# Performance work log

Hardware: AMD Instinct MI355X
Metric: run time of the kernel (lower is better)

## Reference

```python
import jax, jax.numpy as jnp
import numpy as np

N = 50000          # nodes
E = 1600000        # edges (avg degree 32)
D_MODEL = 128      # input == output dim
HEADS = 4
D_HEAD = D_MODEL // HEADS
N_LAYERS = 3


def _edge_softmax(scores, dst, n):
    # scores: [E, H]; softmax over edges sharing the same destination node
    m = jax.ops.segment_max(scores, dst, num_segments=n)          # [N, H]
    m = jnp.where(jnp.isfinite(m), m, 0.0)                        # empty segments -> -inf guard
    ex = jnp.exp(scores - m[dst])                                 # [E, H]
    denom = jax.ops.segment_sum(ex, dst, num_segments=n)          # [N, H]
    return ex / (denom[dst] + 1e-9)


def _gt_layer(h, src, dst, Wq, Wk, Wv, Wo):
    # h: [N, D]; one multi-head graph-attention (graph transformer) layer
    n = h.shape[0]
    q = (h @ Wq).reshape(n, HEADS, D_HEAD)
    k = (h @ Wk).reshape(n, HEADS, D_HEAD)
    v = (h @ Wv).reshape(n, HEADS, D_HEAD)
    scale = 1.0 / np.sqrt(D_HEAD).astype(np.float32)
    scores = jnp.einsum('ehd,ehd->eh', q[dst], k[src]) * scale    # [E, H]
    alpha = _edge_softmax(scores, dst, n)                         # [E, H]
    agg = jax.ops.segment_sum(alpha[:, :, None] * v[src], dst, num_segments=n)  # [N, H, Dh]
    return agg.reshape(n, D_MODEL) @ Wo


def setup_inputs() -> dict:
    key = jax.random.key(0)
    ks = jax.random.split(key, 16)
    s = 1.0 / np.sqrt(D_MODEL)
    inp = {
        'X':    jax.random.normal(ks[0], (N, 1), jnp.float32),
        'Seed': jax.random.uniform(ks[1], (N, 1), jnp.float32),
        'D':    jax.random.uniform(ks[2], (N, 1), jnp.float32),
        'C':    jax.random.uniform(ks[3], (N, 1), jnp.float32),
        'edge_src': jax.random.randint(ks[4], (E,), 0, N, jnp.int32),
        'edge_dst': jax.random.randint(ks[5], (E,), 0, N, jnp.int32),
        # scalar -> d_model embeddings (Linear(1, d, bias=False))
        'W_seed': jax.random.normal(ks[6], (1, D_MODEL), jnp.float32),
        'W_deg':  jax.random.normal(ks[7], (1, D_MODEL), jnp.float32),
        'W_clu':  jax.random.normal(ks[8], (1, D_MODEL), jnp.float32),
        # 3 graph-transformer layers
        'Wq': jax.random.normal(ks[9],  (N_LAYERS, D_MODEL, D_MODEL), jnp.float32) * s,
        'Wk': jax.random.normal(ks[10], (N_LAYERS, D_MODEL, D_MODEL), jnp.float32) * s,
        'Wv': jax.random.normal(ks[11], (N_LAYERS, D_MODEL, D_MODEL), jnp.float32) * s,
        'Wo': jax.random.normal(ks[12], (N_LAYERS, D_MODEL, D_MODEL), jnp.float32) * s,
        # MLP head: Linear(d,d)+ReLU, Linear(d,1)
        'W1': jax.random.normal(ks[13], (D_MODEL, D_MODEL), jnp.float32) * s,
        'b1': jnp.zeros((D_MODEL,), jnp.float32),
        'W2': jax.random.normal(ks[14], (D_MODEL, 1), jnp.float32) * s,
        'b2': jnp.zeros((1,), jnp.float32),
    }
    return inp


def reference(X, Seed, D, C, edge_src, edge_dst,
              W_seed, W_deg, W_clu, Wq, Wk, Wv, Wo, W1, b1, W2, b2):
    # faithful to original: raw X [N,1] broadcast-added to the embeddings
    h = X + Seed @ W_seed + D @ W_deg + C @ W_clu                 # [N, D_MODEL]
    for i in range(N_LAYERS):
        h = _gt_layer(h, edge_src, edge_dst, Wq[i], Wk[i], Wv[i], Wo[i])
    z = jax.nn.relu(h @ W1 + b1)
    return z @ W2 + b2                                            # [N, 1]
```

## Files before the change

### kernel.cpp

```cpp
#include <hip/hip_runtime.h>
#include <math.h>

#define DM 128
#define HEADS 4
#define DH 32
#define WSTRIDE 16384

typedef _Float16 f16x8 __attribute__((ext_vector_type(8)));
typedef _Float16 f16x4 __attribute__((ext_vector_type(4)));
typedef _Float16 f16x2 __attribute__((ext_vector_type(2)));
typedef float f32x4v __attribute__((ext_vector_type(4)));

__device__ __forceinline__ float dpp_xor1_add(float x) {
    int r = __builtin_amdgcn_update_dpp(0, __builtin_bit_cast(int, x), 0xB1, 0xf, 0xf, true);
    return x + __builtin_bit_cast(float, r);
}
__device__ __forceinline__ float dpp_xor2_add(float x) {
    int r = __builtin_amdgcn_update_dpp(0, __builtin_bit_cast(int, x), 0x4E, 0xf, 0xf, true);
    return x + __builtin_bit_cast(float, r);
}

__global__ void embed_kernel(const float* __restrict__ X, const float* __restrict__ Seed,
                             const float* __restrict__ Dg, const float* __restrict__ Cl,
                             const float* __restrict__ Wseed, const float* __restrict__ Wdeg,
                             const float* __restrict__ Wclu, float* __restrict__ H, int n) {
    int i = blockIdx.x * blockDim.x + threadIdx.x;
    if (i >= n * (DM / 4)) return;
    int nd = i >> 5, d4 = (i & 31) * 4;
    float x = X[nd], sd = Seed[nd], dg = Dg[nd], cl = Cl[nd];
    float4 ws = *reinterpret_cast<const float4*>(Wseed + d4);
    float4 wd = *reinterpret_cast<const float4*>(Wdeg + d4);
    float4 wc = *reinterpret_cast<const float4*>(Wclu + d4);
    float4 o;
    o.x = x + sd * ws.x + dg * wd.x + cl * wc.x;
    o.y = x + sd * ws.y + dg * wd.y + cl * wc.y;
    o.z = x + sd * ws.z + dg * wd.z + cl * wc.z;
    o.w = x + sd * ws.w + dg * wd.w + cl * wc.w;
    *reinterpret_cast<float4*>(H + nd * DM + d4) = o;
}

__global__ void count_kernel(const int* __restrict__ edst, int* __restrict__ deg, int E) {
    int e = blockIdx.x * blockDim.x + threadIdx.x;
    if (e < E) atomicAdd(&deg[edst[e]], 1);
}

__global__ void scan1_kernel(const int* __restrict__ in, int* __restrict__ outv,
                             int* __restrict__ bsums, int n) {
    __shared__ int s[256];
    int t = threadIdx.x;
    int i = blockIdx.x * 256 + t;
    int v = (i < n) ? in[i] : 0;
    s[t] = v;
    __syncthreads();
    for (int off = 1; off < 256; off <<= 1) {
        int x = (t >= off) ? s[t - off] : 0;
        __syncthreads();
        s[t] += x;
        __syncthreads();
    }
    if (i < n) outv[i] = s[t];
    if (t == 255) bsums[blockIdx.x] = s[255];
}

__global__ void scan2_kernel(int* __restrict__ bsums, int nb) {
    __shared__ int s[256];
    int t = threadIdx.x;
    int v = (t < nb) ? bsums[t] : 0;
    s[t] = v;
    __syncthreads();
    for (int off = 1; off < 256; off <<= 1) {
        int x = (t >= off) ? s[t - off] : 0;
        __syncthreads();
        s[t] += x;
        __syncthreads();
    }
    if (t < nb) bsums[t] = s[t];
}

__global__ void scan3_kernel(const int* __restrict__ outv, const int* __restrict__ bsums,
                             int* __restrict__ ptr, int n) {
    int i = blockIdx.x * 256 + threadIdx.x;
    if (i == 0) ptr[0] = 0;
    if (i < n) {
        int add = (blockIdx.x > 0) ? bsums[blockIdx.x - 1] : 0;
        ptr[i + 1] = outv[i] + add;
    }
}

__global__ void scatter_kernel(const int* __restrict__ esrc, const int* __restrict__ edst,
                               const int* __restrict__ ptr, int* __restrict__ fill,
                               int* __restrict__ out, int E) {
    int e = blockIdx.x * blockDim.x + threadIdx.x;
    if (e >= E) return;
    int d = edst[e];
    int pos = ptr[d] + atomicAdd(&fill[d], 1);
    out[pos] = esrc[e];
}

__global__ void prepack_kernel(const float* __restrict__ Wq, const float* __restrict__ Wk,
                               const float* __restrict__ Wv, const float* __restrict__ Wo,
                               const float* __restrict__ W1, _Float16* __restrict__ W16) {
    int m = blockIdx.z;
    const float* W;
    if (m < 3)       W = Wq + (size_t)m * DM * DM;
    else if (m < 6)  W = Wk + (size_t)(m - 3) * DM * DM;
    else if (m < 9)  W = Wv + (size_t)(m - 6) * DM * DM;
    else if (m < 12) W = Wo + (size_t)(m - 9) * DM * DM;
    else             W = W1;
    int kb = blockIdx.x, nb = blockIdx.y, l = threadIdx.x;
    int kbase = kb * 32 + (l >> 4) * 8;
    int c = nb * 16 + (l & 15);
    f16x8 v;
#pragma unroll
    for (int j = 0; j < 8; j++) v[j] = (_Float16)W[(kbase + j) * DM + c];
    *reinterpret_cast<f16x8*>(W16 + (size_t)m * WSTRIDE + ((kb * 8 + nb) * 64 + l) * 8) = v;
}

template <int OUT>
__global__ __launch_bounds__(256) void gemm_mfma_kernel(const float* __restrict__ A,
                                                        const _Float16* __restrict__ W16,
                                                        void* __restrict__ O, int ldO,
                                                        int colOff, int n) {
    __shared__ _Float16 sA[64 * 136];
    int t = threadIdx.x;
    int row0 = blockIdx.x * 64;
#pragma unroll
    for (int p = 0; p < 8; p++) {
        int f = p * 256 + t;
        int r = f >> 5, c4 = (f & 31) * 4;
        int gr = min(row0 + r, n - 1);
        float4 v = *reinterpret_cast<const float4*>(A + (size_t)gr * DM + c4);
        f16x4 h = {(_Float16)v.x, (_Float16)v.y, (_Float16)v.z, (_Float16)v.w};
        *reinterpret_cast<f16x4*>(&sA[r * 136 + c4]) = h;
    }
    __syncthreads();

    int w = t >> 6, l = t & 63;
    int lr = l & 15, lg = l >> 4;
    int rowb = w * 16;

    f32x4v acc[8];
#pragma unroll
    for (int nb = 0; nb < 8; nb++) acc[nb] = (f32x4v){0.f, 0.f, 0.f, 0.f};

#pragma unroll
    for (int kb = 0; kb < 4; kb++) {
        f16x8 a = *reinterpret_cast<const f16x8*>(&sA[(rowb + lr) * 136 + kb * 32 + lg * 8]);
#pragma unroll
        for (int nb = 0; nb < 8; nb++) {
            f16x8 b = *reinterpret_cast<const f16x8*>(&W16[((kb * 8 + nb) * 64 + l) * 8]);
            acc[nb] = __builtin_amdgcn_mfma_f32_16x16x32_f16(a, b, acc[nb], 0, 0, 0);
        }
    }

#pragma unroll
    for (int nb = 0; nb < 8; nb++) {
#pragma unroll
        for (int i = 0; i < 4; i++) {
            int r = row0 + rowb + lg * 4 + i;
            if (r >= n) continue;
            int c = nb * 16 + lr;
            if (OUT == 0) {
                ((float*)O)[(size_t)r * ldO + c] = acc[nb][i];
            } else {
                _Float16 h = (_Float16)acc[nb][i];
                ((unsigned short*)O)[(size_t)r * ldO + colOff + c] =
                    __builtin_bit_cast(unsigned short, h);
            }
        }
    }
}

__global__ __launch_bounds__(256) void attn_kernel(const float* __restrict__ Q,
                                                   const uint32_t* __restrict__ KV,
                                                   const int* __restrict__ ptr,
                                                   const int* __restrict__ esrc,
                                                   float* __restrict__ AGG, int n) {
    int wv = threadIdx.x >> 6;
    int lane = threadIdx.x & 63;
    int node = blockIdx.x * 4 + wv;
    if (node >= n) return;
    int e0 = ptr[node], e1 = ptr[node + 1];
    int q4 = lane >> 4;
    int w = lane & 15;
    float* outbase = AGG + (size_t)node * DM + 8 * w;
    if (e0 >= e1) {
        if (lane < 16) {
            *reinterpret_cast<float4*>(outbase) = make_float4(0.f, 0.f, 0.f, 0.f);
            *reinterpret_cast<float4*>(outbase + 4) = make_float4(0.f, 0.f, 0.f, 0.f);
        }
        return;
    }
    const float scale = 0.17677669529663687f * 1.4426950408889634f;
    float4 qa = *reinterpret_cast<const float4*>(Q + (size_t)node * DM + 8 * w);
    float4 qb = *reinterpret_cast<const float4*>(Q + (size_t)node * DM + 8 * w + 4);
    f16x2 qh0 = {(_Float16)(qa.x * scale), (_Float16)(qa.y * scale)};
    f16x2 qh1 = {(_Float16)(qa.z * scale), (_Float16)(qa.w * scale)};
    f16x2 qh2 = {(_Float16)(qb.x * scale), (_Float16)(qb.y * scale)};
    f16x2 qh3 = {(_Float16)(qb.z * scale), (_Float16)(qb.w * scale)};

    float m = -1e30f, s = 0.f;
    float a0 = 0.f, a1 = 0.f, a2 = 0.f, a3 = 0.f, a4 = 0.f, a5 = 0.f, a6 = 0.f, a7 = 0.f;

    int last = e1 - 1;
    int niter = (e1 - e0 + 3) >> 2;
    int niter2 = (niter + 1) >> 1;

    const uint32_t* kvw = KV + w * 4;

    uint4 k0, v0, k1, v1;
    {
        int i0 = esrc[min(e0 + q4, last)];
        const uint32_t* r0 = kvw + (size_t)i0 * 128;
        k0 = *reinterpret_cast<const uint4*>(r0);
        v0 = *reinterpret_cast<const uint4*>(r0 + 64);
        int i1 = esrc[min(e0 + 4 + q4, last)];
        const uint32_t* r1 = kvw + (size_t)i1 * 128;
        k1 = *reinterpret_cast<const uint4*>(r1);
        v1 = *reinterpret_cast<const uint4*>(r1 + 64);
    }
    int idx2 = esrc[min(e0 + 8 + q4, last)];

#define APROC(kc, vc, bidx)                                                            \
    {                                                                                  \
        float p = __builtin_amdgcn_fdot2(qh0, __builtin_bit_cast(f16x2, (kc).x), 0.f, false); \
        p = __builtin_amdgcn_fdot2(qh1, __builtin_bit_cast(f16x2, (kc).y), p, false);  \
        p = __builtin_amdgcn_fdot2(qh2, __builtin_bit_cast(f16x2, (kc).z), p, false);  \
        p = __builtin_amdgcn_fdot2(qh3, __builtin_bit_cast(f16x2, (kc).w), p, false);  \
        p = dpp_xor1_add(p);                                                           \
        p = dpp_xor2_add(p);                                                           \
        p = ((bidx) < e1) ? p : -3.0e38f;                                              \
        float diff = p - m;                                                            \
        if (__any(diff > 8.f)) {                                                       \
            float mn = fmaxf(m, p);                                                    \
            float dd = exp2f(m - mn);                                                  \
            s *= dd;                                                                   \
            a0 *= dd; a1 *= dd; a2 *= dd; a3 *= dd;                                    \
            a4 *= dd; a5 *= dd; a6 *= dd; a7 *= dd;                                    \
            m = mn;                                                                    \
            diff = p - m;                                                              \
        }                                                                              \
        float wg = exp2f(diff);                                                        \
        s += wg;                                                                       \
        f16x2 vh0 = __builtin_bit_cast(f16x2, (vc).x);                                 \
        f16x2 vh1 = __builtin_bit_cast(f16x2, (vc).y);                                 \
        f16x2 vh2 = __builtin_bit_cast(f16x2, (vc).z);                                 \
        f16x2 vh3 = __builtin_bit_cast(f16x2, (vc).w);                                 \
        a0 += wg * (float)vh0[0]; a1 += wg * (float)vh0[1];                            \
        a2 += wg * (float)vh1[0]; a3 += wg * (float)vh1[1];                            \
        a4 += wg * (float)vh2[0]; a5 += wg * (float)vh2[1];                            \
        a6 += wg * (float)vh3[0]; a7 += wg * (float)vh3[1];                            \
    }

    int b = e0 + q4;
    for (int it = 0; it < niter2; it++) {
        {
            uint4 kc = k0, vc = v0;
            const uint32_t* r = kvw + (size_t)idx2 * 128;
            k0 = *reinterpret_cast<const uint4*>(r);
            v0 = *reinterpret_cast<const uint4*>(r + 64);
            idx2 = esrc[min(b + 12, last)];
            APROC(kc, vc, b);
            b += 4;
        }
        {
            uint4 kc = k1, vc = v1;
            const uint32_t* r = kvw + (size_t)idx2 * 128;
            k1 = *reinterpret_cast<const uint4*>(r);
            v1 = *reinterpret_cast<const uint4*>(r + 64);
            idx2 = esrc[min(b + 12, last)];
            APROC(kc, vc, b);
            b += 4;
        }
    }
#undef APROC

#pragma unroll
    for (int off = 16; off <= 32; off <<= 1) {
        float m2 = __shfl_xor(m, off, 64);
        float s2 = __shfl_xor(s, off, 64);
        float b0 = __shfl_xor(a0, off, 64), b1 = __shfl_xor(a1, off, 64);
        float b2 = __shfl_xor(a2, off, 64), b3 = __shfl_xor(a3, off, 64);
        float b4 = __shfl_xor(a4, off, 64), b5 = __shfl_xor(a5, off, 64);
        float b6 = __shfl_xor(a6, off, 64), b7 = __shfl_xor(a7, off, 64);
        float mF = fmaxf(m, m2);
        float d1 = exp2f(m - mF), d2 = exp2f(m2 - mF);
        s = s * d1 + s2 * d2;
        a0 = a0 * d1 + b0 * d2; a1 = a1 * d1 + b1 * d2;
        a2 = a2 * d1 + b2 * d2; a3 = a3 * d1 + b3 * d2;
        a4 = a4 * d1 + b4 * d2; a5 = a5 * d1 + b5 * d2;
        a6 = a6 * d1 + b6 * d2; a7 = a7 * d1 + b7 * d2;
        m = mF;
    }

    float inv = 1.f / (s + 1e-9f);
    if (lane < 16) {
        *reinterpret_cast<float4*>(outbase) =
            make_float4(a0 * inv, a1 * inv, a2 * inv, a3 * inv);
        *reinterpret_cast<float4*>(outbase + 4) =
            make_float4(a4 * inv, a5 * inv, a6 * inv, a7 * inv);
    }
}

__global__ __launch_bounds__(256) void mlp_kernel(const float* __restrict__ H,
                                                  const _Float16* __restrict__ W16,
                                                  const float* __restrict__ b1,
                                                  const float* __restrict__ W2,
                                                  const float* __restrict__ b2,
                                                  float* __restrict__ out, int n) {
    __shared__ _Float16 sA[64 * 136];
    int t = threadIdx.x;
    int row0 = blockIdx.x * 64;
#pragma unroll
    for (int p = 0; p < 8; p++) {
        int f = p * 256 + t;
        int r = f >> 5, c4 = (f & 31) * 4;
        int gr = min(row0 + r, n - 1);
        float4 v = *reinterpret_cast<const float4*>(H + (size_t)gr * DM + c4);
        f16x4 h = {(_Float16)v.x, (_Float16)v.y, (_Float16)v.z, (_Float16)v.w};
        *reinterpret_cast<f16x4*>(&sA[r * 136 + c4]) = h;
    }
    __syncthreads();

    int w = t >> 6, l = t & 63;
    int lr = l & 15, lg = l >> 4;
    int rowb = w * 16;

    f32x4v acc[8];
#pragma unroll
    for (int nb = 0; nb < 8; nb++) acc[nb] = (f32x4v){0.f, 0.f, 0.f, 0.f};

#pragma unroll
    for (int kb = 0; kb < 4; kb++) {
        f16x8 a = *reinterpret_cast<const f16x8*>(&sA[(rowb + lr) * 136 + kb * 32 + lg * 8]);
#pragma unroll
        for (int nb = 0; nb < 8; nb++) {
            f16x8 b = *reinterpret_cast<const f16x8*>(&W16[((kb * 8 + nb) * 64 + l) * 8]);
            acc[nb] = __builtin_amdgcn_mfma_f32_16x16x32_f16(a, b, acc[nb], 0, 0, 0);
        }
    }

    float part[4] = {0.f, 0.f, 0.f, 0.f};
#pragma unroll
    for (int nb = 0; nb < 8; nb++) {
        int c = nb * 16 + lr;
        float b1v = b1[c];
        float w2v = W2[c];
#pragma unroll
        for (int i = 0; i < 4; i++) {
            float z = fmaxf(acc[nb][i] + b1v, 0.f);
            part[i] += z * w2v;
        }
    }
    float b2v = b2[0];
#pragma unroll
    for (int i = 0; i < 4; i++) {
        part[i] += __shfl_xor(part[i], 1, 64);
        part[i] += __shfl_xor(part[i], 2, 64);
        part[i] += __shfl_xor(part[i], 4, 64);
        part[i] += __shfl_xor(part[i], 8, 64);
        int r = row0 + rowb + lg * 4 + i;
        if (lr == 0 && r < n) out[r] = part[i] + b2v;
    }
}

extern "C" void kernel_launch(void* const* d_in, const int* in_sizes, int n_in,
                              void* d_out, int out_size, void* d_ws, size_t ws_size,
                              hipStream_t stream) {
    const float* X    = (const float*)d_in[0];
    const float* Seed = (const float*)d_in[1];
    const float* Dg   = (const float*)d_in[2];
    const float* Cl   = (const float*)d_in[3];
    const int* esrc   = (const int*)d_in[4];
    const int* edst   = (const int*)d_in[5];
    const float* Wseed = (const float*)d_in[6];
    const float* Wdeg  = (const float*)d_in[7];
    const float* Wclu  = (const float*)d_in[8];
    const float* Wq = (const float*)d_in[9];
    const float* Wk = (const float*)d_in[10];
    const float* Wv = (const float*)d_in[11];
    const float* Wo = (const float*)d_in[12];
    const float* W1 = (const float*)d_in[13];
    const float* b1 = (const float*)d_in[14];
    const float* W2 = (const float*)d_in[15];
    const float* b2 = (const float*)d_in[16];
    float* out = (float*)d_out;

    int n = in_sizes[0];
    int E = in_sizes[4];

    char* p = (char*)d_ws;
    auto alloc = [&](size_t bytes) {
        void* r = (void*)p;
        p += (bytes + 255) & ~(size_t)255;
        return r;
    };
    float* hbuf  = (float*)alloc((size_t)n * DM * 4);
    float* qbuf  = (float*)alloc((size_t)n * DM * 4);
    float* abuf  = (float*)alloc((size_t)n * DM * 4);
    unsigned short* kvbuf = (unsigned short*)alloc((size_t)n * 256 * 2);
    _Float16* W16 = (_Float16*)alloc((size_t)13 * WSTRIDE * 2);
    int* deg    = (int*)alloc((size_t)n * 4);
    int* ptr    = (int*)alloc((size_t)(n + 1) * 4);
    int* ptrtmp = (int*)alloc((size_t)n * 4);
    int* bsums  = (int*)alloc(1024);
    int* fill   = (int*)alloc((size_t)n * 4);
    int* esrcs  = (int*)alloc((size_t)E * 4);
    (void)ws_size; (void)n_in; (void)out_size;

    hipMemsetAsync(deg, 0, (size_t)n * 4, stream);
    hipMemsetAsync(fill, 0, (size_t)n * 4, stream);

    {
        int total = n * (DM / 4);
        embed_kernel<<<(total + 255) / 256, 256, 0, stream>>>(X, Seed, Dg, Cl, Wseed, Wdeg,
                                                              Wclu, hbuf, n);
    }
    int nb = (n + 255) / 256;
    count_kernel<<<(E + 255) / 256, 256, 0, stream>>>(edst, deg, E);
    scan1_kernel<<<nb, 256, 0, stream>>>(deg, ptrtmp, bsums, n);
    scan2_kernel<<<1, 256, 0, stream>>>(bsums, nb);
    scan3_kernel<<<nb, 256, 0, stream>>>(ptrtmp, bsums, ptr, n);
    scatter_kernel<<<(E + 255) / 256, 256, 0, stream>>>(esrc, edst, ptr, fill, esrcs, E);

    prepack_kernel<<<dim3(4, 8, 13), 64, 0, stream>>>(Wq, Wk, Wv, Wo, W1, W16);

    int ggrid = (n + 63) / 64;
    int agrid = (n + 3) / 4;
    for (int i = 0; i < 3; i++) {
        const _Float16* wq16 = W16 + (size_t)(0 + i) * WSTRIDE;
        const _Float16* wk16 = W16 + (size_t)(3 + i) * WSTRIDE;
        const _Float16* wv16 = W16 + (size_t)(6 + i) * WSTRIDE;
        const _Float16* wo16 = W16 + (size_t)(9 + i) * WSTRIDE;
        gemm_mfma_kernel<0><<<ggrid, 256, 0, stream>>>(hbuf, wq16, qbuf, DM, 0, n);
        gemm_mfma_kernel<1><<<ggrid, 256, 0, stream>>>(hbuf, wk16, kvbuf, 256, 0, n);
        gemm_mfma_kernel<1><<<ggrid, 256, 0, stream>>>(hbuf, wv16, kvbuf, 256, 128, n);
        attn_kernel<<<agrid, 256, 0, stream>>>(qbuf, (const uint32_t*)kvbuf, ptr, esrcs,
                                               abuf, n);
        gemm_mfma_kernel<0><<<ggrid, 256, 0, stream>>>(abuf, wo16, hbuf, DM, 0, n);
    }
    mlp_kernel<<<ggrid, 256, 0, stream>>>(hbuf, W16 + (size_t)12 * WSTRIDE, b1, W2, b2, out, n);
}
```

Before: 716.9 us.

## Fuse embed/Wo projections with QKV GEMMs and MLP; store activations in fp16

Measured after the change: 670.7 us. -6.5%, faster.

```diff
diff --git a/kernel.cpp b/kernel.cpp
--- a/kernel.cpp
+++ b/kernel.cpp
@@ -19,24 +19,9 @@
     int r = __builtin_amdgcn_update_dpp(0, __builtin_bit_cast(int, x), 0x4E, 0xf, 0xf, true);
     return x + __builtin_bit_cast(float, r);
 }
-
-__global__ void embed_kernel(const float* __restrict__ X, const float* __restrict__ Seed,
-                             const float* __restrict__ Dg, const float* __restrict__ Cl,
-                             const float* __restrict__ Wseed, const float* __restrict__ Wdeg,
-                             const float* __restrict__ Wclu, float* __restrict__ H, int n) {
-    int i = blockIdx.x * blockDim.x + threadIdx.x;
-    if (i >= n * (DM / 4)) return;
-    int nd = i >> 5, d4 = (i & 31) * 4;
-    float x = X[nd], sd = Seed[nd], dg = Dg[nd], cl = Cl[nd];
-    float4 ws = *reinterpret_cast<const float4*>(Wseed + d4);
-    float4 wd = *reinterpret_cast<const float4*>(Wdeg + d4);
-    float4 wc = *reinterpret_cast<const float4*>(Wclu + d4);
-    float4 o;
-    o.x = x + sd * ws.x + dg * wd.x + cl * wc.x;
-    o.y = x + sd * ws.y + dg * wd.y + cl * wc.y;
-    o.z = x + sd * ws.z + dg * wd.z + cl * wc.z;
-    o.w = x + sd * ws.w + dg * wd.w + cl * wc.w;
-    *reinterpret_cast<float4*>(H + nd * DM + d4) = o;
+__device__ __forceinline__ uint32_t pkh(float x, float y) {
+    f16x2 h = {(_Float16)x, (_Float16)y};
+    return __builtin_bit_cast(uint32_t, h);
 }
 
 __global__ void count_kernel(const int* __restrict__ edst, int* __restrict__ deg, int E) {
@@ -116,66 +101,182 @@
     *reinterpret_cast<f16x8*>(W16 + (size_t)m * WSTRIDE + ((kb * 8 + nb) * 64 + l) * 8) = v;
 }
 
-template <int OUT>
-__global__ __launch_bounds__(256) void gemm_mfma_kernel(const float* __restrict__ A,
-                                                        const _Float16* __restrict__ W16,
-                                                        void* __restrict__ O, int ldO,
-                                                        int colOff, int n) {
-    __shared__ _Float16 sA[64 * 136];
+__device__ __forceinline__ void tile_gemm(const _Float16* __restrict__ sRow,
+                                          const _Float16* __restrict__ W16, int lg, int l,
+                                          f32x4v acc[8]) {
+#pragma unroll
+    for (int nb = 0; nb < 8; nb++) acc[nb] = (f32x4v){0.f, 0.f, 0.f, 0.f};
+#pragma unroll
+    for (int kb = 0; kb < 4; kb++) {
+        f16x8 a = *reinterpret_cast<const f16x8*>(sRow + kb * 32 + lg * 8);
+#pragma unroll
+        for (int nb = 0; nb < 8; nb++) {
+            f16x8 b = *reinterpret_cast<const f16x8*>(&W16[((kb * 8 + nb) * 64 + l) * 8]);
+            acc[nb] = __builtin_amdgcn_mfma_f32_16x16x32_f16(a, b, acc[nb], 0, 0, 0);
+        }
+    }
+}
+
+__device__ __forceinline__ void qkv_store(const _Float16* __restrict__ sH, int rowb, int lr,
+                                          int lg, int l, int row0, int n,
+                                          const _Float16* __restrict__ Wq16,
+                                          const _Float16* __restrict__ Wk16,
+                                          const _Float16* __restrict__ Wv16,
+                                          _Float16* __restrict__ Qo,
+                                          _Float16* __restrict__ KVo) {
+    const _Float16* sRow = sH + (rowb + lr) * 136;
+    f32x4v acc[8];
+    tile_gemm(sRow, Wq16, lg, l, acc);
+#pragma unroll
+    for (int nb = 0; nb < 8; nb++)
+#pragma unroll
+        for (int i = 0; i < 4; i++) {
+            int r = row0 + rowb + lg * 4 + i;
+            if (r < n) Qo[(size_t)r * DM + nb * 16 + lr] = (_Float16)acc[nb][i];
+        }
+    tile_gemm(sRow, Wk16, lg, l, acc);
+#pragma unroll
+    for (int nb = 0; nb < 8; nb++)
+#pragma unroll
+        for (int i = 0; i < 4; i++) {
+            int r = row0 + rowb + lg * 4 + i;
+            if (r < n) KVo[(size_t)r * 256 + nb * 16 + lr] = (_Float16)acc[nb][i];
+        }
+    tile_gemm(sRow, Wv16, lg, l, acc);
+#pragma unroll
+    for (int nb = 0; nb < 8; nb++)
+#pragma unroll
+        for (int i = 0; i < 4; i++) {
+            int r = row0 + rowb + lg * 4 + i;
+            if (r < n) KVo[(size_t)r * 256 + 128 + nb * 16 + lr] = (_Float16)acc[nb][i];
+        }
+}
+
+__global__ __launch_bounds__(256) void fused_embed_qkv_kernel(
+    const float* __restrict__ X, const float* __restrict__ Seed,
+    const float* __restrict__ Dg, const float* __restrict__ Cl,
+    const float* __restrict__ Wseed, const float* __restrict__ Wdeg,
+    const float* __restrict__ Wclu,
+    const _Float16* __restrict__ Wq16, const _Float16* __restrict__ Wk16,
+    const _Float16* __restrict__ Wv16,
+    _Float16* __restrict__ Qo, _Float16* __restrict__ KVo, int n) {
+    __shared__ _Float16 sH[64 * 136];
     int t = threadIdx.x;
     int row0 = blockIdx.x * 64;
-#pragma unroll
-    for (int p = 0; p < 8; p++) {
+    {
+        int row = t >> 2, qt = t & 3;
+        int gr = min(row0 + row, n - 1);
+        float x = X[gr], sd = Seed[gr], dg = Dg[gr], cl = Cl[gr];
+#pragma unroll
+        for (int j = 0; j < 8; j++) {
+            int c4 = qt * 32 + j * 4;
+            float4 ws = *reinterpret_cast<const float4*>(Wseed + c4);
+            float4 wd = *reinterpret_cast<const float4*>(Wdeg + c4);
+            float4 wc = *reinterpret_cast<const float4*>(Wclu + c4);
+            f16x4 h;
+            h[0] = (_Float16)(x + sd * ws.x + dg * wd.x + cl * wc.x);
+            h[1] = (_Float16)(x + sd * ws.y + dg * wd.y + cl * wc.y);
+            h[2] = (_Float16)(x + sd * ws.z + dg * wd.z + cl * wc.z);
+            h[3] = (_Float16)(x + sd * ws.w + dg * wd.w + cl * wc.w);
+            *reinterpret_cast<f16x4*>(&sH[row * 136 + c4]) = h;
+        }
+    }
+    __syncthreads();
+    int w = t >> 6, l = t & 63;
+    qkv_store(sH, w * 16, l & 15, l >> 4, l, row0, n, Wq16, Wk16, Wv16, Qo, KVo);
+}
+
+__global__ __launch_bounds__(256) void fused_wo_qkv_kernel(
+    const _Float16* __restrict__ Ain, const _Float16* __restrict__ Wo16,
+    const _Float16* __restrict__ Wq16, const _Float16* __restrict__ Wk16,
+    const _Float16* __restrict__ Wv16,
+    _Float16* __restrict__ Qo, _Float16* __restrict__ KVo, int n) {
+    __shared__ _Float16 sA[64 * 136];
+    __shared__ _Float16 sH[64 * 136];
+    int t = threadIdx.x;
+    int row0 = blockIdx.x * 64;
+#pragma unroll
+    for (int p = 0; p < 4; p++) {
         int f = p * 256 + t;
-        int r = f >> 5, c4 = (f & 31) * 4;
+        int r = f >> 4, c8 = (f & 15) * 8;
         int gr = min(row0 + r, n - 1);
-        float4 v = *reinterpret_cast<const float4*>(A + (size_t)gr * DM + c4);
-        f16x4 h = {(_Float16)v.x, (_Float16)v.y, (_Float16)v.z, (_Float16)v.w};
-        *reinterpret_cast<f16x4*>(&sA[r * 136 + c4]) = h;
-    }
-    __syncthreads();
-
+        *reinterpret_cast<uint4*>(&sA[r * 136 + c8]) =
+            *reinterpret_cast<const uint4*>(Ain + (size_t)gr * DM + c8);
+    }
+    __syncthreads();
     int w = t >> 6, l = t & 63;
     int lr = l & 15, lg = l >> 4;
     int rowb = w * 16;
-
     f32x4v acc[8];
-#pragma unroll
-    for (int nb = 0; nb < 8; nb++) acc[nb] = (f32x4v){0.f, 0.f, 0.f, 0.f};
-
-#pragma unroll
-    for (int kb = 0; kb < 4; kb++) {
-        f16x8 a = *reinterpret_cast<const f16x8*>(&sA[(rowb + lr) * 136 + kb * 32 + lg * 8]);
-#pragma unroll
-        for (int nb = 0; nb < 8; nb++) {
-            f16x8 b = *reinterpret_cast<const f16x8*>(&W16[((kb * 8 + nb) * 64 + l) * 8]);
-            acc[nb] = __builtin_amdgcn_mfma_f32_16x16x32_f16(a, b, acc[nb], 0, 0, 0);
-        }
-    }
-
+    tile_gemm(sA + (rowb + lr) * 136, Wo16, lg, l, acc);
+#pragma unroll
+    for (int nb = 0; nb < 8; nb++)
+#pragma unroll
+        for (int i = 0; i < 4; i++)
+            sH[(rowb + lg * 4 + i) * 136 + nb * 16 + lr] = (_Float16)acc[nb][i];
+    __syncthreads();
+    qkv_store(sH, rowb, lr, lg, l, row0, n, Wq16, Wk16, Wv16, Qo, KVo);
+}
+
+__global__ __launch_bounds__(256) void fused_wo_mlp_kernel(
+    const _Float16* __restrict__ Ain, const _Float16* __restrict__ Wo16,
+    const _Float16* __restrict__ W116, const float* __restrict__ b1,
+    const float* __restrict__ W2, const float* __restrict__ b2,
+    float* __restrict__ out, int n) {
+    __shared__ _Float16 sA[64 * 136];
+    __shared__ _Float16 sH[64 * 136];
+    int t = threadIdx.x;
+    int row0 = blockIdx.x * 64;
+#pragma unroll
+    for (int p = 0; p < 4; p++) {
+        int f = p * 256 + t;
+        int r = f >> 4, c8 = (f & 15) * 8;
+        int gr = min(row0 + r, n - 1);
+        *reinterpret_cast<uint4*>(&sA[r * 136 + c8]) =
+            *reinterpret_cast<const uint4*>(Ain + (size_t)gr * DM + c8);
+    }
+    __syncthreads();
+    int w = t >> 6, l = t & 63;
+    int lr = l & 15, lg = l >> 4;
+    int rowb = w * 16;
+    f32x4v acc[8];
+    tile_gemm(sA + (rowb + lr) * 136, Wo16, lg, l, acc);
+#pragma unroll
+    for (int nb = 0; nb < 8; nb++)
+#pragma unroll
+        for (int i = 0; i < 4; i++)
+            sH[(rowb + lg * 4 + i) * 136 + nb * 16 + lr] = (_Float16)acc[nb][i];
+    __syncthreads();
+    tile_gemm(sH + (rowb + lr) * 136, W116, lg, l, acc);
+    float part[4] = {0.f, 0.f, 0.f, 0.f};
 #pragma unroll
     for (int nb = 0; nb < 8; nb++) {
+        int c = nb * 16 + lr;
+        float b1v = b1[c];
+        float w2v = W2[c];
 #pragma unroll
         for (int i = 0; i < 4; i++) {
-            int r = row0 + rowb + lg * 4 + i;
-            if (r >= n) continue;
-            int c = nb * 16 + lr;
-            if (OUT == 0) {
-                ((float*)O)[(size_t)r * ldO + c] = acc[nb][i];
-            } else {
-                _Float16 h = (_Float16)acc[nb][i];
-                ((unsigned short*)O)[(size_t)r * ldO + colOff + c] =
-                    __builtin_bit_cast(unsigned short, h);
-            }
-        }
-    }
-}
-
-__global__ __launch_bounds__(256) void attn_kernel(const float* __restrict__ Q,
+            float z = fmaxf(acc[nb][i] + b1v, 0.f);
+            part[i] += z * w2v;
+        }
+    }
+    float b2v = b2[0];
+#pragma unroll
+    for (int i = 0; i < 4; i++) {
+        part[i] += __shfl_xor(part[i], 1, 64);
+        part[i] += __shfl_xor(part[i], 2, 64);
+        part[i] += __shfl_xor(part[i], 4, 64);
+        part[i] += __shfl_xor(part[i], 8, 64);
+        int r = row0 + rowb + lg * 4 + i;
+        if (lr == 0 && r < n) out[r] = part[i] + b2v;
+    }
+}
+
+__global__ __launch_bounds__(256) void attn_kernel(const _Float16* __restrict__ Q,
                                                    const uint32_t* __restrict__ KV,
                                                    const int* __restrict__ ptr,
                                                    const int* __restrict__ esrc,
-                                                   float* __restrict__ AGG, int n) {
+                                                   _Float16* __restrict__ AGG, int n) {
     int wv = threadIdx.x >> 6;
     int lane = threadIdx.x & 63;
     int node = blockIdx.x * 4 + wv;
@@ -183,21 +284,17 @@
     int e0 = ptr[node], e1 = ptr[node + 1];
     int q4 = lane >> 4;
     int w = lane & 15;
-    float* outbase = AGG + (size_t)node * DM + 8 * w;
+    _Float16* outbase = AGG + (size_t)node * DM + 8 * w;
     if (e0 >= e1) {
-        if (lane < 16) {
-            *reinterpret_cast<float4*>(outbase) = make_float4(0.f, 0.f, 0.f, 0.f);
-            *reinterpret_cast<float4*>(outbase + 4) = make_float4(0.f, 0.f, 0.f, 0.f);
-        }
+        if (lane < 16) *reinterpret_cast<uint4*>(outbase) = make_uint4(0, 0, 0, 0);
         return;
     }
     const float scale = 0.17677669529663687f * 1.4426950408889634f;
-    float4 qa = *reinterpret_cast<const float4*>(Q + (size_t)node * DM + 8 * w);
-    float4 qb = *reinterpret_cast<const float4*>(Q + (size_t)node * DM + 8 * w + 4);
-    f16x2 qh0 = {(_Float16)(qa.x * scale), (_Float16)(qa.y * scale)};
-    f16x2 qh1 = {(_Float16)(qa.z * scale), (_Float16)(qa.w * scale)};
-    f16x2 qh2 = {(_Float16)(qb.x * scale), (_Float16)(qb.y * scale)};
-    f16x2 qh3 = {(_Float16)(qb.z * scale), (_Float16)(qb.w * scale)};
+    uint4 qv = *reinterpret_cast<const uint4*>(Q + (size_t)node * DM + 8 * w);
+    f16x2 qh0 = __builtin_bit_cast(f16x2, qv.x);
+    f16x2 qh1 = __builtin_bit_cast(f16x2, qv.y);
+    f16x2 qh2 = __builtin_bit_cast(f16x2, qv.z);
+    f16x2 qh3 = __builtin_bit_cast(f16x2, qv.w);
 
     float m = -1e30f, s = 0.f;
     float a0 = 0.f, a1 = 0.f, a2 = 0.f, a3 = 0.f, a4 = 0.f, a5 = 0.f, a6 = 0.f, a7 = 0.f;
@@ -229,6 +326,7 @@
         p = __builtin_amdgcn_fdot2(qh3, __builtin_bit_cast(f16x2, (kc).w), p, false);  \
         p = dpp_xor1_add(p);                                                           \
         p = dpp_xor2_add(p);                                                           \
+        p *= scale;                                                                    \
         p = ((bidx) < e1) ? p : -3.0e38f;                                              \
         float diff = p - m;                                                            \
         if (__any(diff > 8.f)) {                                                       \
@@ -295,72 +393,12 @@
 
     float inv = 1.f / (s + 1e-9f);
     if (lane < 16) {
-        *reinterpret_cast<float4*>(outbase) =
-            make_float4(a0 * inv, a1 * inv, a2 * inv, a3 * inv);
-        *reinterpret_cast<float4*>(outbase + 4) =
-            make_float4(a4 * inv, a5 * inv, a6 * inv, a7 * inv);
-    }
-}
-
-__global__ __launch_bounds__(256) void mlp_kernel(const float* __restrict__ H,
-                                                  const _Float16* __restrict__ W16,
-                                                  const float* __restrict__ b1,
-                                                  const float* __restrict__ W2,
-                                                  const float* __restrict__ b2,
-                                                  float* __restrict__ out, int n) {
-    __shared__ _Float16 sA[64 * 136];
-    int t = threadIdx.x;
-    int row0 = blockIdx.x * 64;
-#pragma unroll
-    for (int p = 0; p < 8; p++) {
-        int f = p * 256 + t;
-        int r = f >> 5, c4 = (f & 31) * 4;
-        int gr = min(row0 + r, n - 1);
-        float4 v = *reinterpret_cast<const float4*>(H + (size_t)gr * DM + c4);
-        f16x4 h = {(_Float16)v.x, (_Float16)v.y, (_Float16)v.z, (_Float16)v.w};
-        *reinterpret_cast<f16x4*>(&sA[r * 136 + c4]) = h;
-    }
-    __syncthreads();
-
-    int w = t >> 6, l = t & 63;
-    int lr = l & 15, lg = l >> 4;
-    int rowb = w * 16;
-
-    f32x4v acc[8];
-#pragma unroll
-    for (int nb = 0; nb < 8; nb++) acc[nb] = (f32x4v){0.f, 0.f, 0.f, 0.f};
-
-#pragma unroll
-    for (int kb = 0; kb < 4; kb++) {
-        f16x8 a = *reinterpret_cast<const f16x8*>(&sA[(rowb + lr) * 136 + kb * 32 + lg * 8]);
-#pragma unroll
-        for (int nb = 0; nb < 8; nb++) {
-            f16x8 b = *reinterpret_cast<const f16x8*>(&W16[((kb * 8 + nb) * 64 + l) * 8]);
-            acc[nb] = __builtin_amdgcn_mfma_f32_16x16x32_f16(a, b, acc[nb], 0, 0, 0);
-        }
-    }
-
-    float part[4] = {0.f, 0.f, 0.f, 0.f};
-#pragma unroll
-    for (int nb = 0; nb < 8; nb++) {
-        int c = nb * 16 + lr;
-        float b1v = b1[c];
-        float w2v = W2[c];
-#pragma unroll
-        for (int i = 0; i < 4; i++) {
-            float z = fmaxf(acc[nb][i] + b1v, 0.f);
-            part[i] += z * w2v;
-        }
-    }
-    float b2v = b2[0];
-#pragma unroll
-    for (int i = 0; i < 4; i++) {
-        part[i] += __shfl_xor(part[i], 1, 64);
-        part[i] += __shfl_xor(part[i], 2, 64);
-        part[i] += __shfl_xor(part[i], 4, 64);
-        part[i] += __shfl_xor(part[i], 8, 64);
-        int r = row0 + rowb + lg * 4 + i;
-        if (lr == 0 && r < n) out[r] = part[i] + b2v;
+        uint4 o;
+        o.x = pkh(a0 * inv, a1 * inv);
+        o.y = pkh(a2 * inv, a3 * inv);
+        o.z = pkh(a4 * inv, a5 * inv);
+        o.w = pkh(a6 * inv, a7 * inv);
+        *reinterpret_cast<uint4*>(outbase) = o;
     }
 }
 
@@ -395,9 +433,8 @@
         p += (bytes + 255) & ~(size_t)255;
         return r;
     };
-    float* hbuf  = (float*)alloc((size_t)n * DM * 4);
-    float* qbuf  = (float*)alloc((size_t)n * DM * 4);
-    float* abuf  = (float*)alloc((size_t)n * DM * 4);
+    _Float16* qbuf = (_Float16*)alloc((size_t)n * DM * 2);
+    _Float16* abuf = (_Float16*)alloc((size_t)n * DM * 2);
     unsigned short* kvbuf = (unsigned short*)alloc((size_t)n * 256 * 2);
     _Float16* W16 = (_Float16*)alloc((size_t)13 * WSTRIDE * 2);
     int* deg    = (int*)alloc((size_t)n * 4);
@@ -411,11 +448,6 @@
     hipMemsetAsync(deg, 0, (size_t)n * 4, stream);
     hipMemsetAsync(fill, 0, (size_t)n * 4, stream);
 
-    {
-        int total = n * (DM / 4);
-        embed_kernel<<<(total + 255) / 256, 256, 0, stream>>>(X, Seed, Dg, Cl, Wseed, Wdeg,
-                                                              Wclu, hbuf, n);
-    }
     int nb = (n + 255) / 256;
     count_kernel<<<(E + 255) / 256, 256, 0, stream>>>(edst, deg, E);
     scan1_kernel<<<nb, 256, 0, stream>>>(deg, ptrtmp, bsums, n);
@@ -427,17 +459,20 @@
 
     int ggrid = (n + 63) / 64;
     int agrid = (n + 3) / 4;
-    for (int i = 0; i < 3; i++) {
-        const _Float16* wq16 = W16 + (size_t)(0 + i) * WSTRIDE;
-        const _Float16* wk16 = W16 + (size_t)(3 + i) * WSTRIDE;
-        const _Float16* wv16 = W16 + (size_t)(6 + i) * WSTRIDE;
-        const _Float16* wo16 = W16 + (size_t)(9 + i) * WSTRIDE;
-        gemm_mfma_kernel<0><<<ggrid, 256, 0, stream>>>(hbuf, wq16, qbuf, DM, 0, n);
-        gemm_mfma_kernel<1><<<ggrid, 256, 0, stream>>>(hbuf, wk16, kvbuf, 256, 0, n);
-        gemm_mfma_kernel<1><<<ggrid, 256, 0, stream>>>(hbuf, wv16, kvbuf, 256, 128, n);
-        attn_kernel<<<agrid, 256, 0, stream>>>(qbuf, (const uint32_t*)kvbuf, ptr, esrcs,
-                                               abuf, n);
-        gemm_mfma_kernel<0><<<ggrid, 256, 0, stream>>>(abuf, wo16, hbuf, DM, 0, n);
-    }
-    mlp_kernel<<<ggrid, 256, 0, stream>>>(hbuf, W16 + (size_t)12 * WSTRIDE, b1, W2, b2, out, n);
-}
+    const _Float16* KVc = (const _Float16*)kvbuf;
+
+    fused_embed_qkv_kernel<<<ggrid, 256, 0, stream>>>(
+        X, Seed, Dg, Cl, Wseed, Wdeg, Wclu,
+        W16 + (size_t)0 * WSTRIDE, W16 + (size_t)3 * WSTRIDE, W16 + (size_t)6 * WSTRIDE,
+        qbuf, (_Float16*)kvbuf, n);
+    attn_kernel<<<agrid, 256, 0, stream>>>(qbuf, (const uint32_t*)KVc, ptr, esrcs, abuf, n);
+    for (int i = 0; i < 2; i++) {
+        fused_wo_qkv_kernel<<<ggrid, 256, 0, stream>>>(
+            abuf, W16 + (size_t)(9 + i) * WSTRIDE,
+            W16 + (size_t)(1 + i) * WSTRIDE, W16 + (size_t)(4 + i) * WSTRIDE,
+            W16 + (size_t)(7 + i) * WSTRIDE, qbuf, (_Float16*)kvbuf, n);
+        attn_kernel<<<agrid, 256, 0, stream>>>(qbuf, (const uint32_t*)KVc, ptr, esrcs, abuf, n);
+    }
+    fused_wo_mlp_kernel<<<ggrid, 256, 0, stream>>>(
+        abuf, W16 + (size_t)11 * WSTRIDE, W16 + (size_t)12 * WSTRIDE, b1, W2, b2, out, n);
+}
```
